# Performance work log

Measured on AMD Instinct MI355X. Metric: run time of the kernel, lower is better.

Reference implementation:

```python
import jax, jax.numpy as jnp
import numpy as np

BLOCK_SIZE = 32
HEADS = 8
DIM_HEAD = 64
ROPE_THETA = 10000.0


def rmsnorm(x, w):
    eps = jnp.finfo(x.dtype).eps
    var = jnp.mean(jnp.square(x), axis=-1, keepdims=True)
    return x * jax.lax.rsqrt(var + eps) * w


def rope_cos_sin(seq_len, dim_head):
    # lucidrains rotary-embedding-torch default: interleaved pairs, theta=10000
    inv_freq = 1.0 / (ROPE_THETA ** (jnp.arange(0, dim_head, 2, dtype=jnp.float32) / dim_head))
    freqs = jnp.arange(seq_len, dtype=jnp.float32)[:, None] * inv_freq[None, :]  # [S, Dh/2]
    return jnp.cos(freqs), jnp.sin(freqs)


def apply_rope(t, cos, sin):
    # t: [B, H, S, Dh], cos/sin: [S, Dh/2]
    t1 = t[..., 0::2]
    t2 = t[..., 1::2]
    out = jnp.stack([t1 * cos - t2 * sin, t1 * sin + t2 * cos], axis=-1)
    return out.reshape(t.shape)


def split_heads(x, h):
    b, n, _ = x.shape
    return x.reshape(b, n, h, -1).transpose(0, 2, 1, 3)  # b h n d


def forward(tokens, attn_norm_w, qkv_w, out_w, mix_w, mix_b,
            ff_norm_w, ff_in_w, ff_in_b, ff_out_w, ff_out_b, final_norm_w):
    B, S, D = tokens.shape
    L = qkv_w.shape[0]
    H, Dh = HEADS, DIM_HEAD
    scale = Dh ** -0.5
    cos, sin = rope_cos_sin(S, Dh)

    # block-causal mask: q_idx // block >= kv_idx // block
    idx = jnp.arange(S)
    allowed = (idx[:, None] // BLOCK_SIZE) >= (idx[None, :] // BLOCK_SIZE)  # [S, S] bool
    neg = -jnp.finfo(tokens.dtype).max

    t = tokens
    first_v = None
    for l in range(L):
        # --- block causal attention ---
        x = rmsnorm(t, attn_norm_w[l])
        qkv = x @ qkv_w[l]  # [B, S, 3*H*Dh]
        q, k, v = jnp.split(qkv, 3, axis=-1)
        q, k, v = split_heads(q, H), split_heads(k, H), split_heads(v, H)  # b h s d
        orig_v = v
        if l > 0:
            mix = jax.nn.sigmoid(x @ mix_w[l] + mix_b[l])  # [B, S, H]
            mix = mix.transpose(0, 2, 1)[..., None]  # [B, H, S, 1]
            v = v + mix * (first_v - v)  # lerp
        q = apply_rope(q, cos, sin)
        k = apply_rope(k, cos, sin)
        sim = jnp.einsum('bhid,bhjd->bhij', q * scale, k)
        sim = jnp.where(allowed, sim, neg)
        attn = jax.nn.softmax(sim, axis=-1)
        o = jnp.einsum('bhij,bhjd->bhid', attn, v)
        o = o.transpose(0, 2, 1, 3).reshape(B, S, H * Dh)
        t = t + o @ out_w[l]
        if first_v is None:
            first_v = orig_v
        # --- SwiGLU feedforward ---
        y = rmsnorm(t, ff_norm_w[l])
        h = y @ ff_in_w[l] + ff_in_b[l]
        a, g = jnp.split(h, 2, axis=-1)
        y = (a * jax.nn.gelu(g, approximate=False)) @ ff_out_w[l] + ff_out_b[l]
        t = t + y

    return rmsnorm(t, final_norm_w)


def setup_inputs():
    key = jax.random.key(0)
    B, S, D, L = 2, 2048, 512, 4
    Di = HEADS * DIM_HEAD  # 512
    Dhid = int(D * 4.0 * 2 / 3)  # 1365
    ks = jax.random.split(key, 8)
    s = 0.02
    return {
        'tokens': jax.random.normal(ks[0], (B, S, D), jnp.float32),
        'attn_norm_w': jnp.ones((L, D), jnp.float32),
        'qkv_w': jax.random.normal(ks[1], (L, D, 3 * Di), jnp.float32) * s,
        'out_w': jax.random.normal(ks[2], (L, Di, D), jnp.float32) * s,
        'mix_w': jax.random.normal(ks[3], (L, D, HEADS), jnp.float32) * s,
        'mix_b': jnp.zeros((L, HEADS), jnp.float32),
        'ff_norm_w': jnp.ones((L, D), jnp.float32),
        'ff_in_w': jax.random.normal(ks[4], (L, D, 2 * Dhid), jnp.float32) * s,
        'ff_in_b': jnp.zeros((L, 2 * Dhid), jnp.float32),
        'ff_out_w': jax.random.normal(ks[5], (L, Dhid, D), jnp.float32) * s,
        'ff_out_b': jnp.zeros((L, D), jnp.float32),
        'final_norm_w': jnp.ones((D,), jnp.float32),
    }


def reference(tokens, attn_norm_w, qkv_w, out_w, mix_w, mix_b,
              ff_norm_w, ff_in_w, ff_in_b, ff_out_w, ff_out_b, final_norm_w):
    return forward(tokens, attn_norm_w, qkv_w, out_w, mix_w, mix_b,
                   ff_norm_w, ff_in_w, ff_in_b, ff_out_w, ff_out_b, final_norm_w)
```

## Files before the change

kernel.cpp:

```cpp
#include <hip/hip_runtime.h>
#include <hip/hip_bf16.h>
#include <math.h>

typedef __bf16 bf16;
typedef bf16 bf16x8 __attribute__((ext_vector_type(8)));
typedef float f32x4 __attribute__((ext_vector_type(4)));

#define LDS16(gp, lp) __builtin_amdgcn_global_load_lds( \
    (const __attribute__((address_space(1))) unsigned int*)(gp), \
    (__attribute__((address_space(3))) unsigned int*)(lp), 16, 0, 0)

__device__ __forceinline__ int cumoff2(int qtp) {
  if (qtp < 4)  return qtp;
  if (qtp < 8)  return 4 + 2 * (qtp - 4);
  if (qtp < 12) return 12 + 3 * (qtp - 8);
  return 24 + 4 * (qtp - 12);
}

__global__ void convert_w_kernel(const float* __restrict__ W, bf16* __restrict__ WT,
                                 int K, int N, int Kp, int Np,
                                 size_t wstride, size_t wtstride)
{
  __shared__ float tile[32][33];
  const float* Wl = W + blockIdx.z * wstride;
  bf16* WTl = WT + blockIdx.z * wtstride;
  int k0 = blockIdx.x * 32, n0 = blockIdx.y * 32;
  int tx = threadIdx.x, ty = threadIdx.y;
  for (int i = ty; i < 32; i += 8) {
    int k = k0 + i, n = n0 + tx;
    tile[i][tx] = (k < K && n < N) ? Wl[(size_t)k * N + n] : 0.f;
  }
  __syncthreads();
  for (int i = ty; i < 32; i += 8) {
    int n = n0 + i, k = k0 + tx;
    if (n < Np && k < Kp) WTl[(size_t)n * Kp + k] = (bf16)tile[tx][i];
  }
}

__global__ void convert_w_ffin_kernel(const float* __restrict__ W, bf16* __restrict__ WT)
{
  __shared__ float tile[32][33];
  const float* Wl = W + (size_t)blockIdx.z * 512 * 2730;
  bf16* WTl = WT + (size_t)blockIdx.z * 2816 * 512;
  int k0 = blockIdx.x * 32, n0 = blockIdx.y * 32;
  int tx = threadIdx.x, ty = threadIdx.y;
  for (int i = ty; i < 32; i += 8) {
    int k = k0 + i, n = n0 + tx;
    int pair = n >> 1;
    int col = (n & 1) ? 1365 + pair : pair;
    tile[i][tx] = (pair < 1365) ? Wl[(size_t)k * 2730 + col] : 0.f;
  }
  __syncthreads();
  for (int i = ty; i < 32; i += 8) {
    int n = n0 + i, k = k0 + tx;
    WTl[(size_t)n * 512 + k] = (bf16)tile[tx][i];
  }
}

__global__ __launch_bounds__(256)
void ibias_kernel(const float* __restrict__ ffib, float* __restrict__ ib)
{
  int idx = blockIdx.x * 256 + threadIdx.x;
  int l = idx / 2816, n = idx - l * 2816;
  int pair = n >> 1;
  int col = (n & 1) ? 1365 + pair : pair;
  ib[idx] = (pair < 1365) ? ffib[l * 2730 + col] : 0.f;
}

__global__ __launch_bounds__(256)
void rope_kernel(float* __restrict__ tab)
{
  int idx = blockIdx.x * 256 + threadIdx.x;
  int s = idx >> 5, j = idx & 31;
  float invf = (float)exp((double)(2 * j) * -0.14391156847064293);
  float ang = (float)s * invf;
  float sn, cs;
  sincosf(ang, &sn, &cs);
  tab[idx] = cs;
  tab[65536 + idx] = sn;
}

template<bool BF16OUT>
__global__ __launch_bounds__(256)
void rmsnorm_kernel(const float* __restrict__ in, const float* __restrict__ wgt,
                    void* __restrict__ outp)
{
  int row = blockIdx.x * 4 + (threadIdx.x >> 6);
  int lane = threadIdx.x & 63;
  const float* p = in + (size_t)row * 512;
  float4 v0 = *(const float4*)(p + lane * 4);
  float4 v1 = *(const float4*)(p + 256 + lane * 4);
  float ss = v0.x*v0.x + v0.y*v0.y + v0.z*v0.z + v0.w*v0.w
           + v1.x*v1.x + v1.y*v1.y + v1.z*v1.z + v1.w*v1.w;
  #pragma unroll
  for (int d = 1; d < 64; d <<= 1) ss += __shfl_xor(ss, d);
  float sc = rsqrtf(ss * (1.f / 512.f) + 1.1920929e-7f);
  float a0[4] = {v0.x, v0.y, v0.z, v0.w};
  float a1[4] = {v1.x, v1.y, v1.z, v1.w};
  #pragma unroll
  for (int i = 0; i < 4; ++i) {
    int c0 = lane * 4 + i, c1 = 256 + lane * 4 + i;
    float r0 = a0[i] * sc * wgt[c0];
    float r1 = a1[i] * sc * wgt[c1];
    if (BF16OUT) {
      ((bf16*)outp)[(size_t)row * 512 + c0] = (bf16)r0;
      ((bf16*)outp)[(size_t)row * 512 + c1] = (bf16)r1;
    } else {
      ((float*)outp)[(size_t)row * 512 + c0] = r0;
      ((float*)outp)[(size_t)row * 512 + c1] = r1;
    }
  }
}

__global__ __launch_bounds__(256)
void qkvpost_kernel(const bf16* __restrict__ qkv, const float* __restrict__ mb,
                    const float* __restrict__ rope, bf16* __restrict__ firstv,
                    bf16* __restrict__ qb, bf16* __restrict__ kb,
                    bf16* __restrict__ vT, int layer)
{
  int idx = blockIdx.x * 256 + threadIdx.x;
  int j = idx & 31;
  int s = (idx >> 5) & 2047;
  int bh = idx >> 16;
  int b = bh >> 3, h = bh & 7;
  size_t row = (size_t)b * 2048 + s;
  const bf16* base = qkv + row * 1664 + h * 64 + 2 * j;
  float q1 = (float)base[0],    q2 = (float)base[1];
  float k1 = (float)base[512],  k2 = (float)base[513];
  float v1 = (float)base[1024], v2 = (float)base[1025];
  float cs = rope[s * 32 + j];
  float sn = rope[65536 + s * 32 + j];
  size_t qoff = ((size_t)bh * 2048 + s) * 64 + 2 * j;
  qb[qoff]     = (bf16)((q1 * cs - q2 * sn) * 0.125f);
  qb[qoff + 1] = (bf16)((q1 * sn + q2 * cs) * 0.125f);
  kb[qoff]     = (bf16)(k1 * cs - k2 * sn);
  kb[qoff + 1] = (bf16)(k1 * sn + k2 * cs);
  if (layer == 0) {
    firstv[qoff] = (bf16)v1; firstv[qoff + 1] = (bf16)v2;
  } else {
    float logit = (float)qkv[row * 1664 + 1536 + h] + mb[h];
    float mx = 1.f / (1.f + __expf(-logit));
    v1 += mx * ((float)firstv[qoff] - v1);
    v2 += mx * ((float)firstv[qoff + 1] - v2);
  }
  vT[((size_t)bh * 64 + 2 * j) * 2048 + s]     = (bf16)v1;
  vT[((size_t)bh * 64 + 2 * j + 1) * 2048 + s] = (bf16)v2;
}

__global__ __launch_bounds__(256, 3)
void attn_kernel(const bf16* __restrict__ Q, const bf16* __restrict__ Kmat,
                 const bf16* __restrict__ VT, bf16* __restrict__ Opart,
                 float* __restrict__ lbuf)
{
  __shared__ __align__(16) bf16 smK[2][8 * 512];
  __shared__ __align__(16) bf16 smV[2][8 * 512];
  __shared__ __align__(16) bf16 smP[4][2][16 * 72];
  const int bid = blockIdx.x;
  const int bh = bid & 15;
  const int cidx = bid >> 4;
  int qtp, chunk;
  if (cidx < 4)       { qtp = cidx; chunk = 0; }
  else if (cidx < 12) { qtp = 4 + ((cidx - 4) >> 1);  chunk = (cidx - 4) & 1; }
  else if (cidx < 24) { int t = cidx - 12; qtp = 8 + t / 3; chunk = t - (qtp - 8) * 3; }
  else                { int t = cidx - 24; qtp = 12 + (t >> 2); chunk = t & 3; }
  const int jt0 = chunk * 8;
  const int njt = min(jt0 + 8, 2 * qtp + 2) - jt0;

  const int tid = threadIdx.x;
  const int w = tid >> 6, lane = tid & 63;
  const int c = lane & 15, quad = lane >> 4;
  const int jtmax_w = (qtp * 4 + w) >> 1;

  const size_t qrow0 = (size_t)bh * 2048 + qtp * 128 + w * 32;
  bf16x8 aQ[2][2];
  #pragma unroll
  for (int m = 0; m < 2; ++m) {
    aQ[m][0] = *(const bf16x8*)(Q + (qrow0 + m * 16 + c) * 64 + quad * 8);
    aQ[m][1] = *(const bf16x8*)(Q + (qrow0 + m * 16 + c) * 64 + 32 + quad * 8);
  }

  const bf16* Kg = Kmat + ((size_t)bh * 2048 + w * 16 + c) * 64 + quad * 8;
  const bf16* Vg = VT + ((size_t)bh * 64 + w * 16 + c) * 2048 + quad * 8;

  {
    const bf16* kp = Kg + (size_t)jt0 * 4096;
    const bf16* vp = Vg + jt0 * 64;
    LDS16(kp,      smK[0] + w * 1024);
    LDS16(kp + 32, smK[0] + w * 1024 + 512);
    LDS16(vp,      smV[0] + w * 1024);
    LDS16(vp + 32, smV[0] + w * 1024 + 512);
  }

  f32x4 o[2][4] = {};
  float lacc[2][4] = {};

  for (int j = 0; j < njt; ++j) {
    const int b = j & 1;
    const int jt = jt0 + j;
    __syncthreads();
    if (j + 1 < njt) {
      const bf16* kp = Kg + (size_t)(jt + 1) * 4096;
      const bf16* vp = Vg + (jt + 1) * 64;
      bf16* kd = smK[1 - b] + w * 1024;
      bf16* vd = smV[1 - b] + w * 1024;
      LDS16(kp,      kd);
      LDS16(kp + 32, kd + 512);
      LDS16(vp,      vd);
      LDS16(vp + 32, vd + 512);
    }
    if (jt > jtmax_w) continue;

    f32x4 s[2][4];
    #pragma unroll
    for (int nt = 0; nt < 4; ++nt) {
      bf16x8 bK0 = *(const bf16x8*)(smK[b] + (nt * 2) * 512 + lane * 8);
      bf16x8 bK1 = *(const bf16x8*)(smK[b] + (nt * 2 + 1) * 512 + lane * 8);
      #pragma unroll
      for (int m = 0; m < 2; ++m) {
        f32x4 acc = {0.f, 0.f, 0.f, 0.f};
        acc = __builtin_amdgcn_mfma_f32_16x16x32_bf16(aQ[m][0], bK0, acc, 0, 0, 0);
        acc = __builtin_amdgcn_mfma_f32_16x16x32_bf16(aQ[m][1], bK1, acc, 0, 0, 0);
        s[m][nt] = acc;
      }
    }
    if (2 * jt + 1 > 4 * qtp + w) {
      #pragma unroll
      for (int m = 0; m < 2; ++m)
        #pragma unroll
        for (int r = 0; r < 4; ++r) { s[m][2][r] = -3.0e38f; s[m][3][r] = -3.0e38f; }
    }

    #pragma unroll
    for (int m = 0; m < 2; ++m) {
      #pragma unroll
      for (int r = 0; r < 4; ++r) {
        float p0 = __expf(s[m][0][r]);
        float p1 = __expf(s[m][1][r]);
        float p2 = __expf(s[m][2][r]);
        float p3 = __expf(s[m][3][r]);
        lacc[m][r] += (p0 + p1) + (p2 + p3);
        bf16* pp = smP[w][m] + (quad * 4 + r) * 72 + c;
        pp[0]  = (bf16)p0;
        pp[16] = (bf16)p1;
        pp[32] = (bf16)p2;
        pp[48] = (bf16)p3;
      }
    }
    asm volatile("s_waitcnt lgkmcnt(0)" ::: "memory");

    #pragma unroll
    for (int ks2 = 0; ks2 < 2; ++ks2) {
      #pragma unroll
      for (int m = 0; m < 2; ++m) {
        bf16x8 aP = *(const bf16x8*)(smP[w][m] + c * 72 + ks2 * 32 + quad * 8);
        #pragma unroll
        for (int nt = 0; nt < 4; ++nt) {
          bf16x8 bV = *(const bf16x8*)(smV[b] + (nt * 2 + ks2) * 512 + lane * 8);
          o[m][nt] = __builtin_amdgcn_mfma_f32_16x16x32_bf16(aP, bV, o[m][nt], 0, 0, 0);
        }
      }
    }
  }

  #pragma unroll
  for (int m = 0; m < 2; ++m)
    #pragma unroll
    for (int r = 0; r < 4; ++r) {
      float v = lacc[m][r];
      #pragma unroll
      for (int d = 1; d < 16; d <<= 1) v += __shfl_xor(v, d);
      lacc[m][r] = v;
    }

  const int slot = bh * 40 + cumoff2(qtp) + chunk;
  bf16* Op = Opart + (size_t)slot * 8192;
  #pragma unroll
  for (int m = 0; m < 2; ++m) {
    #pragma unroll
    for (int r = 0; r < 4; ++r) {
      int prow = w * 32 + m * 16 + quad * 4 + r;
      #pragma unroll
      for (int nt = 0; nt < 4; ++nt)
        Op[prow * 64 + nt * 16 + c] = (bf16)o[m][nt][r];
      if (c == 0) lbuf[slot * 128 + prow] = lacc[m][r];
    }
  }
}

__global__ __launch_bounds__(256)
void attn_combine_kernel(const bf16* __restrict__ Opart, const float* __restrict__ lbuf,
                         bf16* __restrict__ Omat)
{
  const int qt = blockIdx.x, bh = blockIdx.y;
  const int qtp = qt >> 1;
  const int nch = (2 * qtp + 9) >> 3;
  const int base = bh * 40 + cumoff2(qtp);
  const int tid = threadIdx.x;
  const int row = tid >> 2, cg = tid & 3;
  const int prow = (qt & 1) * 64 + row;

  float L = 0.f;
  float acc[16] = {};
  #pragma unroll
  for (int ch = 0; ch < 4; ++ch) {
    if (ch < nch) {
      L += lbuf[(base + ch) * 128 + prow];
      const bf16* p = Opart + (size_t)(base + ch) * 8192 + prow * 64 + cg * 16;
      bf16x8 u0 = *(const bf16x8*)(p);
      bf16x8 u1 = *(const bf16x8*)(p + 8);
      #pragma unroll
      for (int i = 0; i < 8; ++i) { acc[i] += (float)u0[i]; acc[8 + i] += (float)u1[i]; }
    }
  }
  float inv = 1.f / L;

  const int b = bh >> 3, h = bh & 7;
  bf16* op = Omat + ((size_t)b * 2048 + qt * 64 + row) * 512 + h * 64 + cg * 16;
  #pragma unroll
  for (int i = 0; i < 16; ++i)
    op[i] = (bf16)(acc[i] * inv);
}

template<int MODE>
__global__ __launch_bounds__(256, 2)
void gemm_kernel(const bf16* __restrict__ A, const bf16* __restrict__ WT,
                 const float* __restrict__ bias, int n_bias,
                 const float* __restrict__ Tin, void* __restrict__ outp,
                 int K, int N)
{
  __shared__ __align__(16) bf16 smA[8 * 512];
  __shared__ __align__(16) bf16 smB[8 * 512];
  const int tid = threadIdx.x;
  const int w = tid >> 6, lane = tid & 63;
  const int c = lane & 15, quad = lane >> 4;
  const int wy = w >> 1, wx = w & 1;
  const int bm = blockIdx.y * 128, bn = blockIdx.x * 128;

  f32x4 acc[4][4] = {};

  const bf16* Ag0 = A  + (size_t)(bm + (w * 2)     * 16 + c) * K + quad * 8;
  const bf16* Ag1 = A  + (size_t)(bm + (w * 2 + 1) * 16 + c) * K + quad * 8;
  const bf16* Bg0 = WT + (size_t)(bn + (w * 2)     * 16 + c) * K + quad * 8;
  const bf16* Bg1 = WT + (size_t)(bn + (w * 2 + 1) * 16 + c) * K + quad * 8;
  bf16* la0 = smA + (w * 2) * 512;
  bf16* la1 = smA + (w * 2 + 1) * 512;
  bf16* lb0 = smB + (w * 2) * 512;
  bf16* lb1 = smB + (w * 2 + 1) * 512;

  const int NK = K >> 5;
  for (int kk = 0; kk < NK; ++kk) {
    const int ko = kk * 32;
    LDS16(Ag0 + ko, la0);
    LDS16(Ag1 + ko, la1);
    LDS16(Bg0 + ko, lb0);
    LDS16(Bg1 + ko, lb1);
    __syncthreads();
    bf16x8 af[4], bfr[4];
    #pragma unroll
    for (int mt = 0; mt < 4; ++mt)
      af[mt] = *(const bf16x8*)(smA + (wy * 4 + mt) * 512 + lane * 8);
    #pragma unroll
    for (int nt = 0; nt < 4; ++nt)
      bfr[nt] = *(const bf16x8*)(smB + (wx * 4 + nt) * 512 + lane * 8);
    #pragma unroll
    for (int mt = 0; mt < 4; ++mt)
      #pragma unroll
      for (int nt = 0; nt < 4; ++nt)
        acc[mt][nt] = __builtin_amdgcn_mfma_f32_16x16x32_bf16(af[mt], bfr[nt], acc[mt][nt], 0, 0, 0);
    __syncthreads();
  }

  const int r0 = bm + wy * 64;
  const int c0 = bn + wx * 64;
  #pragma unroll
  for (int mt = 0; mt < 4; ++mt) {
    #pragma unroll
    for (int nt = 0; nt < 4; ++nt) {
      #pragma unroll
      for (int r = 0; r < 4; ++r) {
        size_t row = (size_t)(r0 + mt * 16 + quad * 4 + r);
        int col = c0 + nt * 16 + c;
        float v = acc[mt][nt][r];
        if (MODE == 3) {
          v += bias[col];
          float g = __shfl_xor(v, 1);
          if ((c & 1) == 0) {
            float outv = v * 0.5f * g * (1.f + erff(g * 0.70710678118654752f));
            ((bf16*)outp)[row * (size_t)(N >> 1) + (col >> 1)] = (bf16)outv;
          }
        } else {
          float bv = (bias != nullptr && col < n_bias) ? bias[col] : 0.f;
          if (MODE == 2) {
            ((float*)outp)[row * N + col] = Tin[row * N + col] + v + bv;
          } else {
            ((bf16*)outp)[row * N + col] = (bf16)(v + bv);
          }
        }
      }
    }
  }
}

template<int MODE>
__global__ __launch_bounds__(256, 4)
void gemm64_kernel(const bf16* __restrict__ A, const bf16* __restrict__ WT,
                   const float* __restrict__ bias, int n_bias,
                   const float* __restrict__ Tin, void* __restrict__ outp,
                   int K, int N)
{
  __shared__ __align__(16) bf16 smA[4 * 512];
  __shared__ __align__(16) bf16 smB[4 * 512];
  const int tid = threadIdx.x;
  const int w = tid >> 6, lane = tid & 63;
  const int c = lane & 15, quad = lane >> 4;
  const int wy = w >> 1, wx = w & 1;
  const int bm = blockIdx.y * 64, bn = blockIdx.x * 64;

  f32x4 acc[2][2] = {};

  const bf16* Ag = A  + (size_t)(bm + w * 16 + c) * K + quad * 8;
  const bf16* Bg = WT + (size_t)(bn + w * 16 + c) * K + quad * 8;
  bf16* la = smA + w * 512;
  bf16* lb = smB + w * 512;

  const int NK = K >> 5;
  for (int kk = 0; kk < NK; ++kk) {
    const int ko = kk * 32;
    LDS16(Ag + ko, la);
    LDS16(Bg + ko, lb);
    __syncthreads();
    bf16x8 af[2], bfr[2];
    #pragma unroll
    for (int mt = 0; mt < 2; ++mt)
      af[mt] = *(const bf16x8*)(smA + (wy * 2 + mt) * 512 + lane * 8);
    #pragma unroll
    for (int nt = 0; nt < 2; ++nt)
      bfr[nt] = *(const bf16x8*)(smB + (wx * 2 + nt) * 512 + lane * 8);
    #pragma unroll
    for (int mt = 0; mt < 2; ++mt)
      #pragma unroll
      for (int nt = 0; nt < 2; ++nt)
        acc[mt][nt] = __builtin_amdgcn_mfma_f32_16x16x32_bf16(af[mt], bfr[nt], acc[mt][nt], 0, 0, 0);
    __syncthreads();
  }

  const int r0 = bm + wy * 32;
  const int c0 = bn + wx * 32;
  #pragma unroll
  for (int mt = 0; mt < 2; ++mt) {
    #pragma unroll
    for (int nt = 0; nt < 2; ++nt) {
      #pragma unroll
      for (int r = 0; r < 4; ++r) {
        size_t row = (size_t)(r0 + mt * 16 + quad * 4 + r);
        int col = c0 + nt * 16 + c;
        float v = acc[mt][nt][r];
        float bv = (bias != nullptr && col < n_bias) ? bias[col] : 0.f;
        if (MODE == 2) {
          ((float*)outp)[row * N + col] = Tin[row * N + col] + v + bv;
        } else {
          ((bf16*)outp)[row * N + col] = (bf16)(v + bv);
        }
      }
    }
  }
}

extern "C" void kernel_launch(void* const* d_in, const int* in_sizes, int n_in,
                              void* d_out, int out_size, void* d_ws, size_t ws_size,
                              hipStream_t stream)
{
  const float* tokens  = (const float*)d_in[0];
  const float* anw     = (const float*)d_in[1];
  const float* qkvw    = (const float*)d_in[2];
  const float* outw    = (const float*)d_in[3];
  const float* mixw    = (const float*)d_in[4];
  const float* mixbias = (const float*)d_in[5];
  const float* fnw     = (const float*)d_in[6];
  const float* ffiw    = (const float*)d_in[7];
  const float* ffib    = (const float*)d_in[8];
  const float* ffow    = (const float*)d_in[9];
  const float* ffob    = (const float*)d_in[10];
  const float* finw    = (const float*)d_in[11];
  float* outp = (float*)d_out;

  char* ws = (char*)d_ws;
  size_t off = 0;
  auto alloc = [&](size_t bytes) -> char* {
    char* p = ws + off;
    off += (bytes + 255) & ~(size_t)255;
    return p;
  };
  bf16* wtq    = (bf16*)alloc((size_t)4 * 1664 * 512 * 2);
  bf16* wto    = (bf16*)alloc((size_t)4 * 512 * 512 * 2);
  bf16* wtfi   = (bf16*)alloc((size_t)4 * 2816 * 512 * 2);
  bf16* wtfo   = (bf16*)alloc((size_t)4 * 512 * 1408 * 2);
  float* ibias = (float*)alloc((size_t)4 * 2816 * 4);
  float* tbuf  = (float*)alloc((size_t)4096 * 512 * 4);
  bf16* xb     = (bf16*)alloc((size_t)4096 * 512 * 2);
  bf16* yb     = (bf16*)alloc((size_t)4096 * 512 * 2);
  char* qkvraw = alloc((size_t)4096 * 1664 * 2);
  bf16* fv     = (bf16*)alloc((size_t)16 * 2048 * 64 * 2);
  bf16* qb     = (bf16*)alloc((size_t)16 * 2048 * 64 * 2);
  bf16* kbuf   = (bf16*)alloc((size_t)16 * 2048 * 64 * 2);
  bf16* vT     = (bf16*)alloc((size_t)16 * 2048 * 64 * 2);
  bf16* ob     = (bf16*)alloc((size_t)4096 * 512 * 2);
  bf16* actb   = (bf16*)alloc((size_t)4096 * 1408 * 2);
  float* rope  = (float*)alloc((size_t)2 * 65536 * 4);
  float* lbuf  = (float*)alloc((size_t)640 * 128 * 4);
  bf16* qkvbf  = (bf16*)qkvraw;
  bf16* Opart  = (bf16*)qkvraw;

  dim3 tcv(32, 8);
  convert_w_kernel<<<dim3(16, 48, 4), tcv, 0, stream>>>(
      qkvw, wtq, 512, 1536, 512, 1536, (size_t)512 * 1536, (size_t)1664 * 512);
  convert_w_kernel<<<dim3(16, 4, 4), tcv, 0, stream>>>(
      mixw, wtq + (size_t)1536 * 512, 512, 8, 512, 128, (size_t)512 * 8, (size_t)1664 * 512);
  convert_w_kernel<<<dim3(16, 16, 4), tcv, 0, stream>>>(
      outw, wto, 512, 512, 512, 512, (size_t)512 * 512, (size_t)512 * 512);
  convert_w_ffin_kernel<<<dim3(16, 88, 4), tcv, 0, stream>>>(ffiw, wtfi);
  convert_w_kernel<<<dim3(44, 16, 4), tcv, 0, stream>>>(
      ffow, wtfo, 1365, 512, 1408, 512, (size_t)1365 * 512, (size_t)1408 * 512);
  ibias_kernel<<<44, 256, 0, stream>>>(ffib, ibias);
  rope_kernel<<<256, 256, 0, stream>>>(rope);
  hipMemcpyAsync(tbuf, tokens, (size_t)4096 * 512 * 4, hipMemcpyDeviceToDevice, stream);

  for (int l = 0; l < 4; ++l) {
    rmsnorm_kernel<true><<<1024, 256, 0, stream>>>(tbuf, anw + l * 512, xb);
    gemm_kernel<0><<<dim3(13, 32), 256, 0, stream>>>(
        xb, wtq + (size_t)l * 1664 * 512, nullptr, 0, nullptr, qkvbf, 512, 1664);
    qkvpost_kernel<<<4096, 256, 0, stream>>>(qkvbf, mixbias + l * 8, rope, fv, qb, kbuf, vT, l);
    attn_kernel<<<640, 256, 0, stream>>>(qb, kbuf, vT, Opart, lbuf);
    attn_combine_kernel<<<dim3(32, 16), 256, 0, stream>>>(Opart, lbuf, ob);
    gemm64_kernel<2><<<dim3(8, 64), 256, 0, stream>>>(
        ob, wto + (size_t)l * 512 * 512, nullptr, 0, tbuf, tbuf, 512, 512);
    rmsnorm_kernel<true><<<1024, 256, 0, stream>>>(tbuf, fnw + l * 512, yb);
    gemm_kernel<3><<<dim3(22, 32), 256, 0, stream>>>(
        yb, wtfi + (size_t)l * 2816 * 512, ibias + (size_t)l * 2816, 2816, nullptr, actb, 512, 2816);
    gemm64_kernel<2><<<dim3(8, 64), 256, 0, stream>>>(
        actb, wtfo + (size_t)l * 512 * 1408, ffob + (size_t)l * 512, 512, tbuf, tbuf, 1408, 512);
  }
  rmsnorm_kernel<false><<<1024, 256, 0, stream>>>(tbuf, finw, outp);
}
```

Before: 759.0 us.

## Vectorize qkvpost with LDS transpose and triple-buffer attention K/V loads

The qkv post-processing kernel now has each thread handle 16 contiguous head dims with 16-byte vector loads and stores. The V transpose goes through shared memory, so writes to vT are coalesced instead of strided scalar stores. The attention kernel moves from double to triple buffering of K/V tiles, prefetching two tiles ahead and using an explicit vmcnt wait plus barrier in place of __syncthreads. This costs more LDS, so the occupancy hint drops from 3 to 2 blocks per CU.

```diff
diff --git a/kernel.cpp b/kernel.cpp
--- a/kernel.cpp
+++ b/kernel.cpp
@@ -112,48 +112,99 @@
   }
 }
 
-__global__ __launch_bounds__(256)
+__global__ __launch_bounds__(256, 4)
 void qkvpost_kernel(const bf16* __restrict__ qkv, const float* __restrict__ mb,
                     const float* __restrict__ rope, bf16* __restrict__ firstv,
                     bf16* __restrict__ qb, bf16* __restrict__ kb,
                     bf16* __restrict__ vT, int layer)
 {
-  int idx = blockIdx.x * 256 + threadIdx.x;
-  int j = idx & 31;
-  int s = (idx >> 5) & 2047;
-  int bh = idx >> 16;
-  int b = bh >> 3, h = bh & 7;
-  size_t row = (size_t)b * 2048 + s;
-  const bf16* base = qkv + row * 1664 + h * 64 + 2 * j;
-  float q1 = (float)base[0],    q2 = (float)base[1];
-  float k1 = (float)base[512],  k2 = (float)base[513];
-  float v1 = (float)base[1024], v2 = (float)base[1025];
-  float cs = rope[s * 32 + j];
-  float sn = rope[65536 + s * 32 + j];
-  size_t qoff = ((size_t)bh * 2048 + s) * 64 + 2 * j;
-  qb[qoff]     = (bf16)((q1 * cs - q2 * sn) * 0.125f);
-  qb[qoff + 1] = (bf16)((q1 * sn + q2 * cs) * 0.125f);
-  kb[qoff]     = (bf16)(k1 * cs - k2 * sn);
-  kb[qoff + 1] = (bf16)(k1 * sn + k2 * cs);
+  __shared__ float smv[64][65];
+  const int st = blockIdx.x, bh = blockIdx.y;
+  const int b = bh >> 3, h = bh & 7;
+  const int tid = threadIdx.x;
+  const int sl = tid >> 2, dg = tid & 3;
+  const int s = st * 64 + sl;
+  const size_t row = (size_t)b * 2048 + s;
+  const bf16* base = qkv + row * 1664 + h * 64 + dg * 16;
+
+  bf16x8 qv0 = *(const bf16x8*)(base);
+  bf16x8 qv1 = *(const bf16x8*)(base + 8);
+  bf16x8 kv0 = *(const bf16x8*)(base + 512);
+  bf16x8 kv1 = *(const bf16x8*)(base + 520);
+  bf16x8 vv0 = *(const bf16x8*)(base + 1024);
+  bf16x8 vv1 = *(const bf16x8*)(base + 1032);
+
+  float cs8[8], sn8[8];
+  #pragma unroll
+  for (int j = 0; j < 8; ++j) {
+    cs8[j] = rope[s * 32 + dg * 8 + j];
+    sn8[j] = rope[65536 + s * 32 + dg * 8 + j];
+  }
+
+  const size_t qoff = ((size_t)bh * 2048 + s) * 64 + dg * 16;
+  bf16x8 oq0, oq1, ok0, ok1;
+  #pragma unroll
+  for (int p = 0; p < 4; ++p) {
+    float q1 = (float)qv0[2 * p], q2 = (float)qv0[2 * p + 1];
+    float k1 = (float)kv0[2 * p], k2 = (float)kv0[2 * p + 1];
+    oq0[2 * p]     = (bf16)((q1 * cs8[p] - q2 * sn8[p]) * 0.125f);
+    oq0[2 * p + 1] = (bf16)((q1 * sn8[p] + q2 * cs8[p]) * 0.125f);
+    ok0[2 * p]     = (bf16)(k1 * cs8[p] - k2 * sn8[p]);
+    ok0[2 * p + 1] = (bf16)(k1 * sn8[p] + k2 * cs8[p]);
+    float q3 = (float)qv1[2 * p], q4v = (float)qv1[2 * p + 1];
+    float k3 = (float)kv1[2 * p], k4 = (float)kv1[2 * p + 1];
+    oq1[2 * p]     = (bf16)((q3 * cs8[p + 4] - q4v * sn8[p + 4]) * 0.125f);
+    oq1[2 * p + 1] = (bf16)((q3 * sn8[p + 4] + q4v * cs8[p + 4]) * 0.125f);
+    ok1[2 * p]     = (bf16)(k3 * cs8[p + 4] - k4 * sn8[p + 4]);
+    ok1[2 * p + 1] = (bf16)(k3 * sn8[p + 4] + k4 * cs8[p + 4]);
+  }
+  *(bf16x8*)(qb + qoff)     = oq0;
+  *(bf16x8*)(qb + qoff + 8) = oq1;
+  *(bf16x8*)(kb + qoff)     = ok0;
+  *(bf16x8*)(kb + qoff + 8) = ok1;
+
+  float vout[16];
+  #pragma unroll
+  for (int i = 0; i < 8; ++i) { vout[i] = (float)vv0[i]; vout[8 + i] = (float)vv1[i]; }
   if (layer == 0) {
-    firstv[qoff] = (bf16)v1; firstv[qoff + 1] = (bf16)v2;
+    *(bf16x8*)(firstv + qoff)     = vv0;
+    *(bf16x8*)(firstv + qoff + 8) = vv1;
   } else {
     float logit = (float)qkv[row * 1664 + 1536 + h] + mb[h];
     float mx = 1.f / (1.f + __expf(-logit));
-    v1 += mx * ((float)firstv[qoff] - v1);
-    v2 += mx * ((float)firstv[qoff + 1] - v2);
-  }
-  vT[((size_t)bh * 64 + 2 * j) * 2048 + s]     = (bf16)v1;
-  vT[((size_t)bh * 64 + 2 * j + 1) * 2048 + s] = (bf16)v2;
-}
-
-__global__ __launch_bounds__(256, 3)
+    bf16x8 fv0 = *(const bf16x8*)(firstv + qoff);
+    bf16x8 fv1 = *(const bf16x8*)(firstv + qoff + 8);
+    #pragma unroll
+    for (int i = 0; i < 8; ++i) {
+      vout[i]     += mx * ((float)fv0[i] - vout[i]);
+      vout[8 + i] += mx * ((float)fv1[i] - vout[8 + i]);
+    }
+  }
+  #pragma unroll
+  for (int i = 0; i < 16; ++i)
+    smv[sl][dg * 16 + i] = vout[i];
+
+  __syncthreads();
+
+  const int d = tid >> 2, q4 = tid & 3;
+  bf16x8 o0, o1;
+  #pragma unroll
+  for (int i = 0; i < 8; ++i) {
+    o0[i] = (bf16)smv[q4 * 16 + i][d];
+    o1[i] = (bf16)smv[q4 * 16 + 8 + i][d];
+  }
+  bf16* vp = vT + ((size_t)bh * 64 + d) * 2048 + st * 64 + q4 * 16;
+  *(bf16x8*)(vp)     = o0;
+  *(bf16x8*)(vp + 8) = o1;
+}
+
+__global__ __launch_bounds__(256, 2)
 void attn_kernel(const bf16* __restrict__ Q, const bf16* __restrict__ Kmat,
                  const bf16* __restrict__ VT, bf16* __restrict__ Opart,
                  float* __restrict__ lbuf)
 {
-  __shared__ __align__(16) bf16 smK[2][8 * 512];
-  __shared__ __align__(16) bf16 smV[2][8 * 512];
+  __shared__ __align__(16) bf16 smK[3][8 * 512];
+  __shared__ __align__(16) bf16 smV[3][8 * 512];
   __shared__ __align__(16) bf16 smP[4][2][16 * 72];
   const int bid = blockIdx.x;
   const int bh = bid & 15;
@@ -182,39 +233,35 @@
   const bf16* Kg = Kmat + ((size_t)bh * 2048 + w * 16 + c) * 64 + quad * 8;
   const bf16* Vg = VT + ((size_t)bh * 64 + w * 16 + c) * 2048 + quad * 8;
 
-  {
-    const bf16* kp = Kg + (size_t)jt0 * 4096;
-    const bf16* vp = Vg + jt0 * 64;
-    LDS16(kp,      smK[0] + w * 1024);
-    LDS16(kp + 32, smK[0] + w * 1024 + 512);
-    LDS16(vp,      smV[0] + w * 1024);
-    LDS16(vp + 32, smV[0] + w * 1024 + 512);
-  }
+  auto stage = [&](int tile, int buf) {
+    const bf16* kp = Kg + (size_t)tile * 4096;
+    const bf16* vp = Vg + tile * 64;
+    bf16* kd = smK[buf] + w * 1024;
+    bf16* vd = smV[buf] + w * 1024;
+    LDS16(kp,      kd);
+    LDS16(kp + 32, kd + 512);
+    LDS16(vp,      vd);
+    LDS16(vp + 32, vd + 512);
+  };
+  stage(jt0, 0);
+  if (njt > 1) stage(jt0 + 1, 1);
 
   f32x4 o[2][4] = {};
   float lacc[2][4] = {};
 
   for (int j = 0; j < njt; ++j) {
-    const int b = j & 1;
+    const int bufc = j % 3;
     const int jt = jt0 + j;
-    __syncthreads();
-    if (j + 1 < njt) {
-      const bf16* kp = Kg + (size_t)(jt + 1) * 4096;
-      const bf16* vp = Vg + (jt + 1) * 64;
-      bf16* kd = smK[1 - b] + w * 1024;
-      bf16* vd = smV[1 - b] + w * 1024;
-      LDS16(kp,      kd);
-      LDS16(kp + 32, kd + 512);
-      LDS16(vp,      vd);
-      LDS16(vp + 32, vd + 512);
-    }
+    if (j + 1 < njt) asm volatile("s_waitcnt vmcnt(4)\n\ts_barrier" ::: "memory");
+    else             asm volatile("s_waitcnt vmcnt(0)\n\ts_barrier" ::: "memory");
+    if (j + 2 < njt) stage(jt0 + j + 2, (j + 2) % 3);
     if (jt > jtmax_w) continue;
 
     f32x4 s[2][4];
     #pragma unroll
     for (int nt = 0; nt < 4; ++nt) {
-      bf16x8 bK0 = *(const bf16x8*)(smK[b] + (nt * 2) * 512 + lane * 8);
-      bf16x8 bK1 = *(const bf16x8*)(smK[b] + (nt * 2 + 1) * 512 + lane * 8);
+      bf16x8 bK0 = *(const bf16x8*)(smK[bufc] + (nt * 2) * 512 + lane * 8);
+      bf16x8 bK1 = *(const bf16x8*)(smK[bufc] + (nt * 2 + 1) * 512 + lane * 8);
       #pragma unroll
       for (int m = 0; m < 2; ++m) {
         f32x4 acc = {0.f, 0.f, 0.f, 0.f};
@@ -255,7 +302,7 @@
         bf16x8 aP = *(const bf16x8*)(smP[w][m] + c * 72 + ks2 * 32 + quad * 8);
         #pragma unroll
         for (int nt = 0; nt < 4; ++nt) {
-          bf16x8 bV = *(const bf16x8*)(smV[b] + (nt * 2 + ks2) * 512 + lane * 8);
+          bf16x8 bV = *(const bf16x8*)(smV[bufc] + (nt * 2 + ks2) * 512 + lane * 8);
           o[m][nt] = __builtin_amdgcn_mfma_f32_16x16x32_bf16(aP, bV, o[m][nt], 0, 0, 0);
         }
       }
@@ -529,7 +576,7 @@
     rmsnorm_kernel<true><<<1024, 256, 0, stream>>>(tbuf, anw + l * 512, xb);
     gemm_kernel<0><<<dim3(13, 32), 256, 0, stream>>>(
         xb, wtq + (size_t)l * 1664 * 512, nullptr, 0, nullptr, qkvbf, 512, 1664);
-    qkvpost_kernel<<<4096, 256, 0, stream>>>(qkvbf, mixbias + l * 8, rope, fv, qb, kbuf, vT, l);
+    qkvpost_kernel<<<dim3(32, 16), 256, 0, stream>>>(qkvbf, mixbias + l * 8, rope, fv, qb, kbuf, vT, l);
     attn_kernel<<<640, 256, 0, stream>>>(qb, kbuf, vT, Opart, lbuf);
     attn_combine_kernel<<<dim3(32, 16), 256, 0, stream>>>(Opart, lbuf, ob);
     gemm64_kernel<2><<<dim3(8, 64), 256, 0, stream>>>(
```

Result: no change. 770.8 us (+1.6%).
